# Kernel optimization log

Measured on AMD Instinct MI355X. Metric: run time of the kernel, lower is better.

The kernel has to match this reference:

```python
import jax, jax.numpy as jnp
import numpy as np

VLAD_K = 8   # vlad_cluster
GHOST_K = 2  # ghost_cluster
IN_DIM = 512
EPS = 1e-12  # F.normalize eps


def setup_inputs() -> dict:
    key = jax.random.key(0)
    k1, k2, k3, k4 = jax.random.split(key, 4)
    N, C, H, W = 32, IN_DIM, 16, 64
    KG = VLAD_K + GHOST_K
    x = jax.random.normal(k1, (N, C, H, W), dtype=jnp.float32)
    # 1x1 conv weight [KG, C, 1, 1] -> store as [KG, C]; bias [KG]
    conv_w = jax.random.normal(k2, (KG, C), dtype=jnp.float32) * (1.0 / np.sqrt(C))
    conv_b = jax.random.normal(k3, (KG,), dtype=jnp.float32) * 0.01
    centers = jax.random.uniform(k4, (KG, C), dtype=jnp.float32)
    return {"x": x, "conv_w": conv_w, "conv_b": conv_b, "centers": centers}


def reference(x, conv_w, conv_b, centers):
    N, C, H, W = x.shape
    P = H * W
    xf = x.reshape(N, C, P)                                   # [N,C,P]
    # 1x1 conv == per-position matmul over channels
    logits = jnp.einsum('ncp,kc->nkp', xf, conv_w) + conv_b[None, :, None]
    a = jax.nn.softmax(logits, axis=1)                        # softmax over clusters, [N,KG,P]
    # algebraic rewrite of sum_p a*(x - c): (a @ x^T) - (sum_p a) * c
    ax = jnp.einsum('nkp,ncp->nkc', a, xf)                    # [N,KG,C]
    a_sum = a.sum(axis=-1)                                    # [N,KG]
    cluster_res = ax - a_sum[..., None] * centers[None]       # [N,KG,C]
    cluster_res = cluster_res[:, :VLAD_K, :]                  # drop ghost clusters
    norm = jnp.linalg.norm(cluster_res, axis=-1, keepdims=True)
    cluster_res = cluster_res / jnp.maximum(norm, EPS)        # L2 normalize per cluster
    return cluster_res.reshape(N, VLAD_K * C)
```

## Files before the change

kernel.cpp:

```cpp
#include <hip/hip_runtime.h>
#include <math.h>

#define N_    32
#define C_    512
#define P_    1024
#define KG_   10
#define KV_   8
#define PBLK_ 64
#define NPB_  (P_ / PBLK_)
#define PS_   81

__global__ __launch_bounds__(512, 8) void vlad_logits_p(
    const float* __restrict__ x, const float* __restrict__ w,
    float* __restrict__ plg) {
  __shared__ float part[PBLK_ * PS_];
  const int t  = threadIdx.x;
  const int pl = t & 63;
  const int cg = __builtin_amdgcn_readfirstlane(t >> 6);
  const int bx = blockIdx.x;
  const int n  = bx >> 5;
  const int pb = (bx >> 1) & 15;
  const int ch = bx & 1;
  const int p0 = pb * PBLK_;
  const int c0 = ch * 256 + cg * 32;

  const float* xp = x + ((size_t)n * C_ + c0) * P_ + p0 + pl;
  const float* wp = w + c0;

  float acc[KG_];
#pragma unroll
  for (int k = 0; k < KG_; ++k) acc[k] = 0.f;

#pragma unroll 8
  for (int i = 0; i < 32; ++i) {
    const float xv = xp[(size_t)i * P_];
#pragma unroll
    for (int k = 0; k < KG_; ++k) acc[k] += xv * wp[k * C_ + i];
  }

#pragma unroll
  for (int k = 0; k < KG_; ++k) part[pl * PS_ + cg * KG_ + k] = acc[k];
  __syncthreads();

  if (t < 64) {
    const size_t row = (size_t)((n * NPB_ + pb) * 2 + ch) * KG_ * 64;
#pragma unroll
    for (int k = 0; k < KG_; ++k) {
      float s = 0.f;
#pragma unroll
      for (int g = 0; g < 8; ++g) s += part[t * PS_ + g * KG_ + k];
      plg[row + k * 64 + t] = s;
    }
  }
}

__global__ __launch_bounds__(64) void vlad_softmax2(
    const float* __restrict__ plg, const float* __restrict__ bias,
    float* __restrict__ a_ws, float* __restrict__ asum_blk) {
  const int t  = threadIdx.x;
  const int n  = blockIdx.x >> 4;
  const int pb = blockIdx.x & 15;
  const size_t r0 = (size_t)((n * NPB_ + pb) * 2 + 0) * KG_ * 64;
  const size_t r1 = (size_t)((n * NPB_ + pb) * 2 + 1) * KG_ * 64;

  float l[KG_];
  float m = -1e30f;
#pragma unroll
  for (int k = 0; k < KG_; ++k) {
    l[k] = plg[r0 + k * 64 + t] + plg[r1 + k * 64 + t] + bias[k];
    m = fmaxf(m, l[k]);
  }
  float sum = 0.f;
#pragma unroll
  for (int k = 0; k < KG_; ++k) { l[k] = __expf(l[k] - m); sum += l[k]; }
  const float inv = 1.f / sum;
#pragma unroll
  for (int k = 0; k < KV_; ++k) {
    const float a = l[k] * inv;
    a_ws[((size_t)n * KV_ + k) * P_ + pb * PBLK_ + t] = a;
    float s = a;
    s += __shfl_xor(s, 1, 64);  s += __shfl_xor(s, 2, 64);
    s += __shfl_xor(s, 4, 64);  s += __shfl_xor(s, 8, 64);
    s += __shfl_xor(s, 16, 64); s += __shfl_xor(s, 32, 64);
    if (t == 0) asum_blk[(n * NPB_ + pb) * KV_ + k] = s;
  }
}

__global__ __launch_bounds__(256) void vlad_ax2(
    const float* __restrict__ x, const float* __restrict__ a_ws,
    float* __restrict__ axp) {
  const int bx   = blockIdx.x;
  const int n    = bx >> 6;
  const int cb   = (bx >> 1) & 31;
  const int ph   = bx & 1;
  const int lane = threadIdx.x & 63;
  const int wv   = threadIdx.x >> 6;
  const int c0   = cb * 16 + wv * 4;

  const float* ap = a_ws + (size_t)n * KV_ * P_ + ph * 512;
  const float* xp = x + (size_t)n * C_ * P_ + ph * 512;

  float acc[4][8];
#pragma unroll
  for (int cc = 0; cc < 4; ++cc)
#pragma unroll
    for (int k = 0; k < 8; ++k) acc[cc][k] = 0.f;

#pragma unroll
  for (int i = 0; i < 2; ++i) {
    const int pb = i * 256 + lane * 4;
    float4 a4[8];
#pragma unroll
    for (int k = 0; k < 8; ++k)
      a4[k] = *reinterpret_cast<const float4*>(ap + (size_t)k * P_ + pb);
#pragma unroll
    for (int cc = 0; cc < 4; ++cc) {
      float4 x4 = *reinterpret_cast<const float4*>(xp + (size_t)(c0 + cc) * P_ + pb);
#pragma unroll
      for (int k = 0; k < 8; ++k)
        acc[cc][k] += x4.x * a4[k].x + x4.y * a4[k].y
                    + x4.z * a4[k].z + x4.w * a4[k].w;
    }
  }

  float v[32];
#pragma unroll
  for (int cc = 0; cc < 4; ++cc)
#pragma unroll
    for (int k = 0; k < 8; ++k) v[cc * 8 + k] = acc[cc][k];

  {  const bool hi = lane & 1;
#pragma unroll
    for (int j = 0; j < 16; ++j) {
      float send = hi ? v[j] : v[j + 16];
      float keep = hi ? v[j + 16] : v[j];
      v[j] = keep + __shfl_xor(send, 1, 64);
    } }
  {  const bool hi = lane & 2;
#pragma unroll
    for (int j = 0; j < 8; ++j) {
      float send = hi ? v[j] : v[j + 8];
      float keep = hi ? v[j + 8] : v[j];
      v[j] = keep + __shfl_xor(send, 2, 64);
    } }
  {  const bool hi = lane & 4;
#pragma unroll
    for (int j = 0; j < 4; ++j) {
      float send = hi ? v[j] : v[j + 4];
      float keep = hi ? v[j + 4] : v[j];
      v[j] = keep + __shfl_xor(send, 4, 64);
    } }
  {  const bool hi = lane & 8;
#pragma unroll
    for (int j = 0; j < 2; ++j) {
      float send = hi ? v[j] : v[j + 2];
      float keep = hi ? v[j + 2] : v[j];
      v[j] = keep + __shfl_xor(send, 8, 64);
    } }
  {  const bool hi = lane & 16;
    float send = hi ? v[0] : v[1];
    float keep = hi ? v[1] : v[0];
    v[0] = keep + __shfl_xor(send, 16, 64);
  }
  v[0] += __shfl_xor(v[0], 32, 64);

  if (lane < 32) {
    const int o = ((lane & 1) << 4) | ((lane & 2) << 2) | (lane & 4)
                | (((lane >> 3) & 1) << 1) | ((lane >> 4) & 1);
    const int cc = o >> 3;
    const int k  = o & 7;
    axp[((size_t)(n * 2 + ph) * KV_ + k) * C_ + (c0 + cc)] = v[0];
  }
}

__global__ __launch_bounds__(256) void vlad_fin(
    const float* __restrict__ axp, const float* __restrict__ asum_blk,
    const float* __restrict__ centers, float* __restrict__ out) {
  __shared__ float sred[4];
  const int n = blockIdx.x >> 3;
  const int k = blockIdx.x & 7;
  const int t = threadIdx.x, lane = t & 63, wv = t >> 6;

  float asv = 0.f;
#pragma unroll
  for (int pb = 0; pb < NPB_; ++pb)
    asv += asum_blk[(n * NPB_ + pb) * KV_ + k];

  const int c = t * 2;
  const float2 a0 = *reinterpret_cast<const float2*>(
      &axp[((size_t)(n * 2 + 0) * KV_ + k) * C_ + c]);
  const float2 a1 = *reinterpret_cast<const float2*>(
      &axp[((size_t)(n * 2 + 1) * KV_ + k) * C_ + c]);
  const float2 ct = *reinterpret_cast<const float2*>(&centers[k * C_ + c]);
  const float r0 = (a0.x + a1.x) - asv * ct.x;
  const float r1 = (a0.y + a1.y) - asv * ct.y;

  float ss = r0 * r0 + r1 * r1;
#pragma unroll
  for (int d = 1; d < 64; d <<= 1) ss += __shfl_xor(ss, d, 64);
  if (lane == 0) sred[wv] = ss;
  __syncthreads();
  const float tot = (sred[0] + sred[1]) + (sred[2] + sred[3]);
  const float inv = 1.f / fmaxf(sqrtf(tot), 1e-12f);

  out[(size_t)n * (KV_ * C_) + k * C_ + c]     = r0 * inv;
  out[(size_t)n * (KV_ * C_) + k * C_ + c + 1] = r1 * inv;
}

extern "C" void kernel_launch(void* const* d_in, const int* in_sizes, int n_in,
                              void* d_out, int out_size, void* d_ws, size_t ws_size,
                              hipStream_t stream) {
  const float* x       = (const float*)d_in[0];
  const float* conv_w  = (const float*)d_in[1];
  const float* conv_b  = (const float*)d_in[2];
  const float* centers = (const float*)d_in[3];
  float* out = (float*)d_out;

  float* plg      = (float*)d_ws;
  float* a_ws     = plg + (size_t)N_ * NPB_ * 2 * KG_ * 64;
  float* axp      = a_ws + (size_t)N_ * KV_ * P_;
  float* asum_blk = axp + (size_t)2 * N_ * KV_ * C_;

  hipLaunchKernelGGL(vlad_logits_p, dim3(N_ * 32), dim3(512), 0, stream,
                     x, conv_w, plg);
  hipLaunchKernelGGL(vlad_softmax2, dim3(N_ * NPB_), dim3(64), 0, stream,
                     plg, conv_b, a_ws, asum_blk);
  hipLaunchKernelGGL(vlad_ax2,     dim3(N_ * 64), dim3(256), 0, stream,
                     x, a_ws, axp);
  hipLaunchKernelGGL(vlad_fin,     dim3(N_ * KV_), dim3(256), 0, stream,
                     axp, asum_blk, centers, out);
}
```

Baseline: 125.6 us.

## Drop P-split in ax kernel, widen softmax blocks, vectorize final store

The ax kernel no longer splits the spatial dimension into two halves. Each block now loops over all 1024 positions and writes a single partial, so the final kernel reads one ax buffer instead of summing two. The softmax kernel now runs 256-thread blocks covering four position tiles each, and the final output store is vectorized to float2. This cuts workspace traffic and block count, at the cost of halving the ax grid (1024 blocks) and giving each block twice the serial work, which may reduce latency hiding.

```diff
diff --git a/kernel.cpp b/kernel.cpp
--- a/kernel.cpp
+++ b/kernel.cpp
@@ -14,17 +14,17 @@
     const float* __restrict__ x, const float* __restrict__ w,
     float* __restrict__ plg) {
   __shared__ float part[PBLK_ * PS_];
-  const int t  = threadIdx.x;
-  const int pl = t & 63;
-  const int cg = __builtin_amdgcn_readfirstlane(t >> 6);
-  const int bx = blockIdx.x;
-  const int n  = bx >> 5;
-  const int pb = (bx >> 1) & 15;
-  const int ch = bx & 1;
-  const int p0 = pb * PBLK_;
-  const int c0 = ch * 256 + cg * 32;
-
-  const float* xp = x + ((size_t)n * C_ + c0) * P_ + p0 + pl;
+  const int t    = threadIdx.x;
+  const int lane = t & 63;
+  const int cg   = __builtin_amdgcn_readfirstlane(t >> 6);
+  const int bx   = blockIdx.x;
+  const int n    = bx >> 5;
+  const int pb   = (bx >> 1) & 15;
+  const int ch   = bx & 1;
+  const int p0   = pb * PBLK_;
+  const int c0   = ch * 256 + cg * 32;
+
+  const float* xp = x + ((size_t)n * C_ + c0) * P_ + p0 + lane;
   const float* wp = w + c0;
 
   float acc[KG_];
@@ -39,7 +39,7 @@
   }
 
 #pragma unroll
-  for (int k = 0; k < KG_; ++k) part[pl * PS_ + cg * KG_ + k] = acc[k];
+  for (int k = 0; k < KG_; ++k) part[lane * PS_ + cg * KG_ + k] = acc[k];
   __syncthreads();
 
   if (t < 64) {
@@ -54,12 +54,17 @@
   }
 }
 
-__global__ __launch_bounds__(64) void vlad_softmax2(
+__global__ __launch_bounds__(256) void vlad_softmax2(
     const float* __restrict__ plg, const float* __restrict__ bias,
     float* __restrict__ a_ws, float* __restrict__ asum_blk) {
   const int t  = threadIdx.x;
-  const int n  = blockIdx.x >> 4;
-  const int pb = blockIdx.x & 15;
+  const int n  = blockIdx.x >> 2;
+  const int pq = blockIdx.x & 3;
+  const int p  = pq * 256 + t;
+  const int pb = p >> 6;
+  const int pl = p & 63;
+  const int lane = t & 63;
+
   const size_t r0 = (size_t)((n * NPB_ + pb) * 2 + 0) * KG_ * 64;
   const size_t r1 = (size_t)((n * NPB_ + pb) * 2 + 1) * KG_ * 64;
 
@@ -67,7 +72,7 @@
   float m = -1e30f;
 #pragma unroll
   for (int k = 0; k < KG_; ++k) {
-    l[k] = plg[r0 + k * 64 + t] + plg[r1 + k * 64 + t] + bias[k];
+    l[k] = plg[r0 + k * 64 + pl] + plg[r1 + k * 64 + pl] + bias[k];
     m = fmaxf(m, l[k]);
   }
   float sum = 0.f;
@@ -77,28 +82,26 @@
 #pragma unroll
   for (int k = 0; k < KV_; ++k) {
     const float a = l[k] * inv;
-    a_ws[((size_t)n * KV_ + k) * P_ + pb * PBLK_ + t] = a;
+    a_ws[((size_t)n * KV_ + k) * P_ + p] = a;
     float s = a;
     s += __shfl_xor(s, 1, 64);  s += __shfl_xor(s, 2, 64);
     s += __shfl_xor(s, 4, 64);  s += __shfl_xor(s, 8, 64);
     s += __shfl_xor(s, 16, 64); s += __shfl_xor(s, 32, 64);
-    if (t == 0) asum_blk[(n * NPB_ + pb) * KV_ + k] = s;
-  }
-}
-
-__global__ __launch_bounds__(256) void vlad_ax2(
+    if (lane == 0) asum_blk[(n * NPB_ + pb) * KV_ + k] = s;
+  }
+}
+
+__global__ __launch_bounds__(256) void vlad_ax(
     const float* __restrict__ x, const float* __restrict__ a_ws,
-    float* __restrict__ axp) {
-  const int bx   = blockIdx.x;
-  const int n    = bx >> 6;
-  const int cb   = (bx >> 1) & 31;
-  const int ph   = bx & 1;
+    float* __restrict__ ax_ws) {
+  const int n    = blockIdx.x >> 5;
+  const int cb   = blockIdx.x & 31;
   const int lane = threadIdx.x & 63;
   const int wv   = threadIdx.x >> 6;
   const int c0   = cb * 16 + wv * 4;
 
-  const float* ap = a_ws + (size_t)n * KV_ * P_ + ph * 512;
-  const float* xp = x + (size_t)n * C_ * P_ + ph * 512;
+  const float* ap = a_ws + (size_t)n * KV_ * P_;
+  const float* xp = x + (size_t)n * C_ * P_;
 
   float acc[4][8];
 #pragma unroll
@@ -107,7 +110,7 @@
     for (int k = 0; k < 8; ++k) acc[cc][k] = 0.f;
 
 #pragma unroll
-  for (int i = 0; i < 2; ++i) {
+  for (int i = 0; i < 4; ++i) {
     const int pb = i * 256 + lane * 4;
     float4 a4[8];
 #pragma unroll
@@ -169,12 +172,12 @@
                 | (((lane >> 3) & 1) << 1) | ((lane >> 4) & 1);
     const int cc = o >> 3;
     const int k  = o & 7;
-    axp[((size_t)(n * 2 + ph) * KV_ + k) * C_ + (c0 + cc)] = v[0];
+    ax_ws[((size_t)n * KV_ + k) * C_ + (c0 + cc)] = v[0];
   }
 }
 
 __global__ __launch_bounds__(256) void vlad_fin(
-    const float* __restrict__ axp, const float* __restrict__ asum_blk,
+    const float* __restrict__ ax_ws, const float* __restrict__ asum_blk,
     const float* __restrict__ centers, float* __restrict__ out) {
   __shared__ float sred[4];
   const int n = blockIdx.x >> 3;
@@ -187,13 +190,11 @@
     asv += asum_blk[(n * NPB_ + pb) * KV_ + k];
 
   const int c = t * 2;
-  const float2 a0 = *reinterpret_cast<const float2*>(
-      &axp[((size_t)(n * 2 + 0) * KV_ + k) * C_ + c]);
-  const float2 a1 = *reinterpret_cast<const float2*>(
-      &axp[((size_t)(n * 2 + 1) * KV_ + k) * C_ + c]);
+  const float2 av = *reinterpret_cast<const float2*>(
+      &ax_ws[((size_t)n * KV_ + k) * C_ + c]);
   const float2 ct = *reinterpret_cast<const float2*>(&centers[k * C_ + c]);
-  const float r0 = (a0.x + a1.x) - asv * ct.x;
-  const float r1 = (a0.y + a1.y) - asv * ct.y;
+  const float r0 = av.x - asv * ct.x;
+  const float r1 = av.y - asv * ct.y;
 
   float ss = r0 * r0 + r1 * r1;
 #pragma unroll
@@ -203,8 +204,10 @@
   const float tot = (sred[0] + sred[1]) + (sred[2] + sred[3]);
   const float inv = 1.f / fmaxf(sqrtf(tot), 1e-12f);
 
-  out[(size_t)n * (KV_ * C_) + k * C_ + c]     = r0 * inv;
-  out[(size_t)n * (KV_ * C_) + k * C_ + c + 1] = r1 * inv;
+  float2 o;
+  o.x = r0 * inv;
+  o.y = r1 * inv;
+  *reinterpret_cast<float2*>(&out[(size_t)n * (KV_ * C_) + k * C_ + c]) = o;
 }
 
 extern "C" void kernel_launch(void* const* d_in, const int* in_sizes, int n_in,
@@ -218,15 +221,15 @@
 
   float* plg      = (float*)d_ws;
   float* a_ws     = plg + (size_t)N_ * NPB_ * 2 * KG_ * 64;
-  float* axp      = a_ws + (size_t)N_ * KV_ * P_;
-  float* asum_blk = axp + (size_t)2 * N_ * KV_ * C_;
+  float* ax_ws    = a_ws + (size_t)N_ * KV_ * P_;
+  float* asum_blk = ax_ws + (size_t)N_ * KV_ * C_;
 
   hipLaunchKernelGGL(vlad_logits_p, dim3(N_ * 32), dim3(512), 0, stream,
                      x, conv_w, plg);
-  hipLaunchKernelGGL(vlad_softmax2, dim3(N_ * NPB_), dim3(64), 0, stream,
+  hipLaunchKernelGGL(vlad_softmax2, dim3(N_ * 4),  dim3(256), 0, stream,
                      plg, conv_b, a_ws, asum_blk);
-  hipLaunchKernelGGL(vlad_ax2,     dim3(N_ * 64), dim3(256), 0, stream,
-                     x, a_ws, axp);
-  hipLaunchKernelGGL(vlad_fin,     dim3(N_ * KV_), dim3(256), 0, stream,
-                     axp, asum_blk, centers, out);
-}
+  hipLaunchKernelGGL(vlad_ax,       dim3(N_ * 32), dim3(256), 0, stream,
+                     x, a_ws, ax_ws);
+  hipLaunchKernelGGL(vlad_fin,      dim3(N_ * KV_), dim3(256), 0, stream,
+                     ax_ws, asum_blk, centers, out);
+}
```

Measured after the change: 129.0 us. 2.7% more time.
